# Optimization experiments

Hardware: AMD Instinct MI355X
Metric: run time of the kernel (lower is better)

Reference implementation:

```python
import jax, jax.numpy as jnp
import numpy as np

SHIFTS = [1, 3, 5, 7]
C = 16  # in_channels // 4
# -1 neighbor offsets for tmp1..tmp8 (dy, dx) in units of the dilation
OFFSETS = [(-1, -1), (-1, 0), (-1, 1), (0, 1), (1, 1), (1, 0), (1, -1), (0, -1)]


def setup_inputs() -> dict:
    key = jax.random.key(0)
    ks = jax.random.split(key, 32)
    d = {}
    d['cen'] = jax.random.normal(ks[0], (8, 64, 256, 256), jnp.float32)
    d['mas'] = jax.random.normal(ks[1], (8, 1, 256, 256), jnp.float32)
    d['in_conv_w'] = jax.random.normal(ks[2], (16, 64), jnp.float32) * 0.1
    d['in_conv_b'] = jax.random.normal(ks[3], (16,), jnp.float32) * 0.1
    for i, s in enumerate(SHIFTS):
        d[f'dw_w{s}'] = jax.random.normal(ks[4 + 2 * i], (16, 1, s, s), jnp.float32) * 0.1
        d[f'dw_b{s}'] = jax.random.normal(ks[5 + 2 * i], (16,), jnp.float32) * 0.1
    d['l1_w'] = jax.random.normal(ks[12], (4, 16, 4), jnp.float32) * 0.1
    d['l1_b'] = jax.random.normal(ks[13], (4, 16), jnp.float32) * 0.1
    d['l2_w'] = jax.random.normal(ks[14], (4, 16, 8), jnp.float32) * 0.1
    d['l2_b'] = jax.random.normal(ks[15], (4, 16), jnp.float32) * 0.1
    d['base_w'] = jax.random.normal(ks[16], (16, 4), jnp.float32) * 0.1
    d['bn_scale'] = jnp.ones((16,), jnp.float32)
    d['bn_bias'] = jnp.zeros((16,), jnp.float32)
    d['final_w'] = jax.random.normal(ks[17], (1, 16), jnp.float32) * 0.1
    d['final_b'] = jax.random.normal(ks[18], (1,), jnp.float32) * 0.1
    return d


def _dw_conv(x, w, b, pad):
    # depthwise conv, groups == channels
    y = jax.lax.conv_general_dilated(
        x, w, window_strides=(1, 1), padding=[(pad, pad), (pad, pad)],
        dimension_numbers=('NCHW', 'OIHW', 'NCHW'), feature_group_count=x.shape[1])
    return y + b[None, :, None, None]


def _shifted(x, dy, dx, d):
    # zero-padded shift: out(y,x) = in(y+dy, x+dx)
    H, W = x.shape[2], x.shape[3]
    p = jnp.pad(x, ((0, 0), (0, 0), (d, d), (d, d)))
    return p[:, :, d + dy:d + dy + H, d + dx:d + dx + W]


def _circ_shift(x, dw_w, dw_b, w1, b1, w2, b2, shift):
    x = _dw_conv(x, dw_w, dw_b, shift // 2)
    # tmp_k = x - x shifted by the k-th neighbor offset (dilation = shift)
    T = [x - _shifted(x, dy * shift, dx * shift, shift) for dy, dx in OFFSETS]
    # paired sums: S[k] = tmp_{k+1} + tmp_{k+5} (S repeats with period 4)
    S = [T[k] + T[k + 4] for k in range(4)]
    outs = []
    for k in range(8):  # fixed small structural loop
        feats = jnp.stack([S[(k + 1) % 4], S[(k + 3) % 4], S[(k + 2) % 4],
                           2.0 * T[(k + 4) % 8]], axis=2)  # (B,C,4,H,W)
        # grouped 1x1 conv (groups=C, 4C->C) == per-channel contraction over feature axis
        o = jnp.einsum('bcfhw,cf->bchw', feats, w1) + b1[None, :, None, None]
        outs.append(o * T[k])
    O = jnp.sort(jnp.stack(outs, axis=2), axis=2)  # (B,C,8,H,W) sorted over branch axis
    return jnp.einsum('bcfhw,cf->bchw', O, w2) + b2[None, :, None, None]


def reference(cen, mas, in_conv_w, in_conv_b, dw_w1, dw_b1, dw_w3, dw_b3,
              dw_w5, dw_b5, dw_w7, dw_b7, l1_w, l1_b, l2_w, l2_b,
              base_w, bn_scale, bn_bias, final_w, final_b):
    # in_conv: 1x1, in_channels -> C
    x = jnp.einsum('bihw,oi->bohw', cen, in_conv_w) + in_conv_b[None, :, None, None]
    dws = [(dw_w1, dw_b1), (dw_w3, dw_b3), (dw_w5, dw_b5), (dw_w7, dw_b7)]
    branches = [
        _circ_shift(x, dws[i][0], dws[i][1], l1_w[i], l1_b[i], l2_w[i], l2_b[i], SHIFTS[i])
        for i in range(len(SHIFTS))
    ]
    A = jnp.sort(jnp.stack(branches, axis=2), axis=2)  # (B,C,4,H,W)
    # out_conv: grouped 1x1 BaseConv (conv no-bias + BN(affine) + SiLU), then 1x1 -> 1, sigmoid
    y = jnp.einsum('bcfhw,cf->bchw', A, base_w)
    y = jax.nn.silu(y * bn_scale[None, :, None, None] + bn_bias[None, :, None, None])
    y = jnp.einsum('bchw,oc->bohw', y, final_w) + final_b[None, :, None, None]
    return jax.nn.sigmoid(y)
```

## Files before the change

### kernel.cpp

```cpp
#include <hip/hip_runtime.h>
#include <hip/hip_fp16.h>
#include <math.h>

#define HW 65536

typedef float v2f __attribute__((ext_vector_type(2), aligned(4)));
typedef _Float16 h2 __attribute__((ext_vector_type(2)));

__global__ __launch_bounds__(256, 8) void k_inconv(const float* __restrict__ cen,
                                                   const float* __restrict__ w,
                                                   const float* __restrict__ bias,
                                                   float* __restrict__ x) {
    int px = blockIdx.x * 256 + threadIdx.x;
    int b  = px >> 16;
    int hw = px & 65535;

    const float* src = cen + (long)(b * 64) * HW + hw;
    float acc[16];
#pragma unroll
    for (int o = 0; o < 16; o++) acc[o] = bias[o];

#pragma unroll 4
    for (int i = 0; i < 64; i++) {
        float v = src[(long)i * HW];
#pragma unroll
        for (int o = 0; o < 16; o++) acc[o] = fmaf(v, w[o * 64 + i], acc[o]);
    }
    float* dst = x + (long)(b * 16) * HW + hw;
#pragma unroll
    for (int o = 0; o < 16; o++) dst[(long)o * HW] = acc[o];
}

#define CEH(a, b) { h2 _t = __builtin_elementwise_min(a, b); \
                    b = __builtin_elementwise_max(a, b); a = _t; }

__device__ __forceinline__ void sort8_h2(h2* v) {
    CEH(v[0], v[1]); CEH(v[2], v[3]); CEH(v[4], v[5]); CEH(v[6], v[7]);
    CEH(v[0], v[2]); CEH(v[1], v[3]); CEH(v[4], v[6]); CEH(v[5], v[7]);
    CEH(v[1], v[2]); CEH(v[5], v[6]); CEH(v[0], v[4]); CEH(v[3], v[7]);
    CEH(v[1], v[5]); CEH(v[2], v[6]);
    CEH(v[1], v[4]); CEH(v[3], v[6]);
    CEH(v[2], v[4]); CEH(v[3], v[5]);
    CEH(v[3], v[4]);
}
__device__ __forceinline__ void sort4_h2(h2* v) {
    CEH(v[0], v[1]); CEH(v[2], v[3]); CEH(v[0], v[2]); CEH(v[1], v[3]); CEH(v[1], v[2]);
}

#define LXS 56
#define SS  48

__global__ __launch_bounds__(512, 4) void k_main(
    const float* __restrict__ x,
    const float* __restrict__ dw_w1, const float* __restrict__ dw_b1,
    const float* __restrict__ dw_w3, const float* __restrict__ dw_b3,
    const float* __restrict__ dw_w5, const float* __restrict__ dw_b5,
    const float* __restrict__ dw_w7, const float* __restrict__ dw_b7,
    const float* __restrict__ l1w, const float* __restrict__ l1b,
    const float* __restrict__ l2w, const float* __restrict__ l2b,
    const float* __restrict__ bw,  const float* __restrict__ bns,
    const float* __restrict__ bnb, __half* __restrict__ y16) {

    const int plane = blockIdx.y;
    const int c     = plane & 15;
    const int ty0   = (blockIdx.x >> 3) * 32;
    const int tx0   = (blockIdx.x & 7) * 32;
    const int tid   = threadIdx.x;

    __shared__ float lx[52 * LXS];
    __shared__ float lxs[4][46 * SS];

    const float* xp = x + (long)plane * HW;

    for (int i = tid; i < 52 * 52; i += 512) {
        int r  = i / 52;
        int cc = i - r * 52;
        int gy = ty0 - 10 + r, gx = tx0 - 10 + cc;
        float v = 0.f;
        if ((unsigned)gy < 256u && (unsigned)gx < 256u) v = xp[gy * 256 + gx];
        lx[r * LXS + cc] = v;
    }
    __syncthreads();

    const float* W7 = dw_w7 + c * 49;
    const float* W5 = dw_w5 + c * 25;
    const float* W3 = dw_w3 + c * 9;
    const float  W1 = dw_w1[c];
    const float  B1 = dw_b1[c], B3 = dw_b3[c], B5 = dw_b5[c], B7 = dw_b7[c];

    for (int u = tid; u < 46 * 23; u += 512) {
        int row = u / 23;
        int pc0 = (u - row * 23) * 2;
        v2f c7 = {0, 0}, c5 = {0, 0}, c3 = {0, 0}, c1 = {0, 0};
#pragma unroll
        for (int a = 0; a < 7; a++) {
            const float* rp = &lx[(row + a) * LXS + pc0];
            v2f q0 = *(const v2f*)rp;
            v2f q1 = *(const v2f*)(rp + 2);
            v2f q2 = *(const v2f*)(rp + 4);
            v2f q3 = *(const v2f*)(rp + 6);
            float v8 = rp[8];
            float v[9] = {q0.x, q0.y, q1.x, q1.y, q2.x, q2.y, q3.x, q3.y, v8};
#pragma unroll
            for (int bb = 0; bb < 7; bb++) {
                v2f vv = {v[bb], v[bb + 1]};
                c7 += vv * W7[a * 7 + bb];
            }
            if (a >= 1 && a <= 5) {
#pragma unroll
                for (int bb = 0; bb < 5; bb++) {
                    v2f vv = {v[bb + 1], v[bb + 2]};
                    c5 += vv * W5[(a - 1) * 5 + bb];
                }
            }
            if (a >= 2 && a <= 4) {
#pragma unroll
                for (int bb = 0; bb < 3; bb++) {
                    v2f vv = {v[bb + 2], v[bb + 3]};
                    c3 += vv * W3[(a - 2) * 3 + bb];
                }
            }
            if (a == 3) {
                v2f vv = {v[3], v[4]};
                c1 = vv * W1;
            }
        }
        int gy  = ty0 - 7 + row;
        int gx0 = tx0 - 7 + pc0;
        bool rin = ((unsigned)gy < 256u);
        bool in0 = rin && ((unsigned)gx0 < 256u);
        bool in1 = rin && ((unsigned)(gx0 + 1) < 256u);
        int o = row * SS + pc0;
        v2f s;
        s.x = in0 ? c1.x + B1 : 0.f; s.y = in1 ? c1.y + B1 : 0.f;
        *(v2f*)&lxs[0][o] = s;
        s.x = in0 ? c3.x + B3 : 0.f; s.y = in1 ? c3.y + B3 : 0.f;
        *(v2f*)&lxs[1][o] = s;
        s.x = in0 ? c5.x + B5 : 0.f; s.y = in1 ? c5.y + B5 : 0.f;
        *(v2f*)&lxs[2][o] = s;
        s.x = in0 ? c7.x + B7 : 0.f; s.y = in1 ? c7.y + B7 : 0.f;
        *(v2f*)&lxs[3][o] = s;
    }
    __syncthreads();

    const int ty  = tid >> 4;
    const int tx2 = (tid & 15) * 2;
    const int gy  = ty0 + ty, gx = tx0 + tx2;
    const int corner = ty * SS + tx2;

    v2f br[4];
#pragma unroll
    for (int i = 0; i < 4; i++) {
        const int s = 1 + 2 * i;
        const float* xs = lxs[i];
        v2f ctr = *(const v2f*)&xs[corner + 7 * SS + 7];
        v2f n0  = *(const v2f*)&xs[corner + (7 - s) * SS + (7 - s)];
        v2f n1  = *(const v2f*)&xs[corner + (7 - s) * SS + 7];
        v2f n2  = *(const v2f*)&xs[corner + (7 - s) * SS + (7 + s)];
        v2f n3  = *(const v2f*)&xs[corner + 7 * SS + (7 + s)];
        v2f n4  = *(const v2f*)&xs[corner + (7 + s) * SS + (7 + s)];
        v2f n5  = *(const v2f*)&xs[corner + (7 + s) * SS + 7];
        v2f n6  = *(const v2f*)&xs[corner + (7 + s) * SS + (7 - s)];
        v2f n7  = *(const v2f*)&xs[corner + 7 * SS + (7 - s)];

        v2f T[8];
        T[0] = ctr - n0; T[1] = ctr - n1; T[2] = ctr - n2; T[3] = ctr - n3;
        T[4] = ctr - n4; T[5] = ctr - n5; T[6] = ctr - n6; T[7] = ctr - n7;
        v2f S[4];
#pragma unroll
        for (int k = 0; k < 4; k++) S[k] = T[k] + T[k + 4];

        const float w10   = l1w[i * 64 + c * 4 + 0];
        const float w11   = l1w[i * 64 + c * 4 + 1];
        const float w12   = l1w[i * 64 + c * 4 + 2];
        const float w13x2 = 2.f * l1w[i * 64 + c * 4 + 3];
        const float bb1   = l1b[i * 16 + c];

        v2f R[4];
#pragma unroll
        for (int m = 0; m < 4; m++) {
            v2f r = S[(m + 2) & 3] * w12 + bb1;
            r = S[(m + 3) & 3] * w11 + r;
            r = S[(m + 1) & 3] * w10 + r;
            R[m] = r;
        }

        h2 h8[8];
#pragma unroll
        for (int k = 0; k < 8; k++) {
            v2f o = (T[(k + 4) & 7] * w13x2 + R[k & 3]) * T[k];
            h8[k] = __builtin_convertvector(o, h2);
        }
        sort8_h2(h8);

        v2f acc = {l2b[i * 16 + c], l2b[i * 16 + c]};
#pragma unroll
        for (int k = 0; k < 8; k++) {
            v2f ov = __builtin_convertvector(h8[k], v2f);
            acc += ov * l2w[i * 128 + c * 8 + k];
        }
        br[i] = acc;
    }

    h2 bh[4];
#pragma unroll
    for (int i = 0; i < 4; i++) bh[i] = __builtin_convertvector(br[i], h2);
    sort4_h2(bh);

    v2f yv = {0.f, 0.f};
#pragma unroll
    for (int i = 0; i < 4; i++) {
        v2f bv = __builtin_convertvector(bh[i], v2f);
        yv += bv * bw[c * 4 + i];
    }
    const float bsc = bns[c], bbi = bnb[c];
    float zx = fmaf(yv.x, bsc, bbi);
    float zy = fmaf(yv.y, bsc, bbi);
    float sx = zx / (1.f + __expf(-zx));
    float sy = zy / (1.f + __expf(-zy));
    *(__half2*)&y16[(long)plane * HW + gy * 256 + gx] = __floats2half2_rn(sx, sy);
}

__global__ __launch_bounds__(256) void k_final(const __half* __restrict__ y16,
                                               const float* __restrict__ fw,
                                               const float* __restrict__ fb,
                                               float* __restrict__ out) {
    long t  = (long)blockIdx.x * 256 + threadIdx.x;
    long p0 = t * 2;
    int  b  = (int)(p0 >> 16);
    int  hw = (int)(p0 & 65535);

    float accx = fb[0], accy = fb[0];
#pragma unroll
    for (int cc = 0; cc < 16; cc++) {
        __half2 h = *(const __half2*)(y16 + (long)(b * 16 + cc) * HW + hw);
        float2 v = __half22float2(h);
        float wv = fw[cc];
        accx = fmaf(v.x, wv, accx);
        accy = fmaf(v.y, wv, accy);
    }
    float2 r;
    r.x = 1.f / (1.f + __expf(-accx));
    r.y = 1.f / (1.f + __expf(-accy));
    *(float2*)(out + p0) = r;
}

extern "C" void kernel_launch(void* const* d_in, const int* in_sizes, int n_in,
                              void* d_out, int out_size, void* d_ws, size_t ws_size,
                              hipStream_t stream) {
    (void)in_sizes; (void)n_in; (void)out_size; (void)ws_size;
    const float* cen   = (const float*)d_in[0];
    const float* in_w  = (const float*)d_in[2];
    const float* in_b  = (const float*)d_in[3];
    const float* dw_w1 = (const float*)d_in[4];
    const float* dw_b1 = (const float*)d_in[5];
    const float* dw_w3 = (const float*)d_in[6];
    const float* dw_b3 = (const float*)d_in[7];
    const float* dw_w5 = (const float*)d_in[8];
    const float* dw_b5 = (const float*)d_in[9];
    const float* dw_w7 = (const float*)d_in[10];
    const float* dw_b7 = (const float*)d_in[11];
    const float* l1w   = (const float*)d_in[12];
    const float* l1b   = (const float*)d_in[13];
    const float* l2w   = (const float*)d_in[14];
    const float* l2b   = (const float*)d_in[15];
    const float* bw    = (const float*)d_in[16];
    const float* bns   = (const float*)d_in[17];
    const float* bnb   = (const float*)d_in[18];
    const float* fw    = (const float*)d_in[19];
    const float* fb    = (const float*)d_in[20];

    float*  xbuf = (float*)d_ws;
    __half* y16  = (__half*)(xbuf + (size_t)8 * 16 * HW);
    float*  out  = (float*)d_out;

    k_inconv<<<2048, 256, 0, stream>>>(cen, in_w, in_b, xbuf);
    k_main<<<dim3(64, 128), 512, 0, stream>>>(xbuf, dw_w1, dw_b1, dw_w3, dw_b3,
                                              dw_w5, dw_b5, dw_w7, dw_b7,
                                              l1w, l1b, l2w, l2b, bw, bns, bnb, y16);
    k_final<<<1024, 256, 0, stream>>>(y16, fw, fb, out);
}
```

Baseline: 394.4 us.

## Store intermediates in fp16 and run circ-shift math in packed half

```diff
diff --git a/kernel.cpp b/kernel.cpp
--- a/kernel.cpp
+++ b/kernel.cpp
@@ -7,28 +7,40 @@
 typedef float v2f __attribute__((ext_vector_type(2), aligned(4)));
 typedef _Float16 h2 __attribute__((ext_vector_type(2)));
 
-__global__ __launch_bounds__(256, 8) void k_inconv(const float* __restrict__ cen,
-                                                   const float* __restrict__ w,
-                                                   const float* __restrict__ bias,
-                                                   float* __restrict__ x) {
-    int px = blockIdx.x * 256 + threadIdx.x;
-    int b  = px >> 16;
-    int hw = px & 65535;
-
-    const float* src = cen + (long)(b * 64) * HW + hw;
-    float acc[16];
-#pragma unroll
-    for (int o = 0; o < 16; o++) acc[o] = bias[o];
+__global__ __launch_bounds__(256) void k_inconv(const float* __restrict__ cen,
+                                                const float* __restrict__ w,
+                                                const float* __restrict__ bias,
+                                                __half* __restrict__ xh) {
+    long t  = (long)blockIdx.x * 256 + threadIdx.x;
+    long p0 = t * 4;
+    int  b  = (int)(p0 >> 16);
+    int  hw = (int)(p0 & 65535);
+
+    const float4* src = (const float4*)(cen + ((long)b * 64) * HW + hw);
+    float4 acc[16];
+#pragma unroll
+    for (int o = 0; o < 16; o++) { float bv = bias[o]; acc[o] = make_float4(bv, bv, bv, bv); }
 
 #pragma unroll 4
     for (int i = 0; i < 64; i++) {
-        float v = src[(long)i * HW];
-#pragma unroll
-        for (int o = 0; o < 16; o++) acc[o] = fmaf(v, w[o * 64 + i], acc[o]);
-    }
-    float* dst = x + (long)(b * 16) * HW + hw;
-#pragma unroll
-    for (int o = 0; o < 16; o++) dst[(long)o * HW] = acc[o];
+        float4 v = src[(long)i * (HW / 4)];
+#pragma unroll
+        for (int o = 0; o < 16; o++) {
+            float wv = w[o * 64 + i];
+            acc[o].x = fmaf(v.x, wv, acc[o].x);
+            acc[o].y = fmaf(v.y, wv, acc[o].y);
+            acc[o].z = fmaf(v.z, wv, acc[o].z);
+            acc[o].w = fmaf(v.w, wv, acc[o].w);
+        }
+    }
+#pragma unroll
+    for (int o = 0; o < 16; o++) {
+        __half2 lo = __floats2half2_rn(acc[o].x, acc[o].y);
+        __half2 hi = __floats2half2_rn(acc[o].z, acc[o].w);
+        __half2* dst = (__half2*)(xh + ((long)(b * 16 + o)) * HW + hw);
+        dst[0] = lo;
+        dst[1] = hi;
+    }
 }
 
 #define CEH(a, b) { h2 _t = __builtin_elementwise_min(a, b); \
@@ -50,8 +62,8 @@
 #define LXS 56
 #define SS  48
 
-__global__ __launch_bounds__(512, 4) void k_main(
-    const float* __restrict__ x,
+__global__ __launch_bounds__(512, 8) void k_main(
+    const __half* __restrict__ xh,
     const float* __restrict__ dw_w1, const float* __restrict__ dw_b1,
     const float* __restrict__ dw_w3, const float* __restrict__ dw_b3,
     const float* __restrict__ dw_w5, const float* __restrict__ dw_b5,
@@ -67,17 +79,17 @@
     const int tx0   = (blockIdx.x & 7) * 32;
     const int tid   = threadIdx.x;
 
-    __shared__ float lx[52 * LXS];
-    __shared__ float lxs[4][46 * SS];
-
-    const float* xp = x + (long)plane * HW;
+    __shared__ float   lx[52 * LXS];
+    __shared__ _Float16 lxs[4][46 * SS];
+
+    const __half* xp = xh + (long)plane * HW;
 
     for (int i = tid; i < 52 * 52; i += 512) {
         int r  = i / 52;
         int cc = i - r * 52;
         int gy = ty0 - 10 + r, gx = tx0 - 10 + cc;
         float v = 0.f;
-        if ((unsigned)gy < 256u && (unsigned)gx < 256u) v = xp[gy * 256 + gx];
+        if ((unsigned)gy < 256u && (unsigned)gx < 256u) v = __half2float(xp[gy * 256 + gx]);
         lx[r * LXS + cc] = v;
     }
     __syncthreads();
@@ -133,13 +145,13 @@
         int o = row * SS + pc0;
         v2f s;
         s.x = in0 ? c1.x + B1 : 0.f; s.y = in1 ? c1.y + B1 : 0.f;
-        *(v2f*)&lxs[0][o] = s;
+        *(h2*)&lxs[0][o] = __builtin_convertvector(s, h2);
         s.x = in0 ? c3.x + B3 : 0.f; s.y = in1 ? c3.y + B3 : 0.f;
-        *(v2f*)&lxs[1][o] = s;
+        *(h2*)&lxs[1][o] = __builtin_convertvector(s, h2);
         s.x = in0 ? c5.x + B5 : 0.f; s.y = in1 ? c5.y + B5 : 0.f;
-        *(v2f*)&lxs[2][o] = s;
+        *(h2*)&lxs[2][o] = __builtin_convertvector(s, h2);
         s.x = in0 ? c7.x + B7 : 0.f; s.y = in1 ? c7.y + B7 : 0.f;
-        *(v2f*)&lxs[3][o] = s;
+        *(h2*)&lxs[3][o] = __builtin_convertvector(s, h2);
     }
     __syncthreads();
 
@@ -148,74 +160,74 @@
     const int gy  = ty0 + ty, gx = tx0 + tx2;
     const int corner = ty * SS + tx2;
 
-    v2f br[4];
+    h2 brh[4];
 #pragma unroll
     for (int i = 0; i < 4; i++) {
         const int s = 1 + 2 * i;
-        const float* xs = lxs[i];
-        v2f ctr = *(const v2f*)&xs[corner + 7 * SS + 7];
-        v2f n0  = *(const v2f*)&xs[corner + (7 - s) * SS + (7 - s)];
-        v2f n1  = *(const v2f*)&xs[corner + (7 - s) * SS + 7];
-        v2f n2  = *(const v2f*)&xs[corner + (7 - s) * SS + (7 + s)];
-        v2f n3  = *(const v2f*)&xs[corner + 7 * SS + (7 + s)];
-        v2f n4  = *(const v2f*)&xs[corner + (7 + s) * SS + (7 + s)];
-        v2f n5  = *(const v2f*)&xs[corner + (7 + s) * SS + 7];
-        v2f n6  = *(const v2f*)&xs[corner + (7 + s) * SS + (7 - s)];
-        v2f n7  = *(const v2f*)&xs[corner + 7 * SS + (7 - s)];
-
-        v2f T[8];
+        const _Float16* xs = lxs[i];
+        h2 ctr = *(const h2*)&xs[corner + 7 * SS + 7];
+        h2 n0  = *(const h2*)&xs[corner + (7 - s) * SS + (7 - s)];
+        h2 n1  = *(const h2*)&xs[corner + (7 - s) * SS + 7];
+        h2 n2  = *(const h2*)&xs[corner + (7 - s) * SS + (7 + s)];
+        h2 n3  = *(const h2*)&xs[corner + 7 * SS + (7 + s)];
+        h2 n4  = *(const h2*)&xs[corner + (7 + s) * SS + (7 + s)];
+        h2 n5  = *(const h2*)&xs[corner + (7 + s) * SS + 7];
+        h2 n6  = *(const h2*)&xs[corner + (7 + s) * SS + (7 - s)];
+        h2 n7  = *(const h2*)&xs[corner + 7 * SS + (7 - s)];
+
+        h2 T[8];
         T[0] = ctr - n0; T[1] = ctr - n1; T[2] = ctr - n2; T[3] = ctr - n3;
         T[4] = ctr - n4; T[5] = ctr - n5; T[6] = ctr - n6; T[7] = ctr - n7;
-        v2f S[4];
+        h2 S[4];
 #pragma unroll
         for (int k = 0; k < 4; k++) S[k] = T[k] + T[k + 4];
 
-        const float w10   = l1w[i * 64 + c * 4 + 0];
-        const float w11   = l1w[i * 64 + c * 4 + 1];
-        const float w12   = l1w[i * 64 + c * 4 + 2];
-        const float w13x2 = 2.f * l1w[i * 64 + c * 4 + 3];
-        const float bb1   = l1b[i * 16 + c];
-
-        v2f R[4];
+        const _Float16 w10   = (_Float16)l1w[i * 64 + c * 4 + 0];
+        const _Float16 w11   = (_Float16)l1w[i * 64 + c * 4 + 1];
+        const _Float16 w12   = (_Float16)l1w[i * 64 + c * 4 + 2];
+        const _Float16 w13x2 = (_Float16)(2.f * l1w[i * 64 + c * 4 + 3]);
+        const _Float16 bb1   = (_Float16)l1b[i * 16 + c];
+
+        const h2 vw10 = {w10, w10}, vw11 = {w11, w11}, vw12 = {w12, w12};
+        const h2 vw13 = {w13x2, w13x2}, vbb1 = {bb1, bb1};
+
+        h2 R[4];
 #pragma unroll
         for (int m = 0; m < 4; m++) {
-            v2f r = S[(m + 2) & 3] * w12 + bb1;
-            r = S[(m + 3) & 3] * w11 + r;
-            r = S[(m + 1) & 3] * w10 + r;
+            h2 r = S[(m + 2) & 3] * vw12 + vbb1;
+            r = S[(m + 3) & 3] * vw11 + r;
+            r = S[(m + 1) & 3] * vw10 + r;
             R[m] = r;
         }
 
         h2 h8[8];
 #pragma unroll
+        for (int k = 0; k < 8; k++)
+            h8[k] = (T[(k + 4) & 7] * vw13 + R[k & 3]) * T[k];
+        sort8_h2(h8);
+
+        _Float16 l2bh = (_Float16)l2b[i * 16 + c];
+        h2 acc = {l2bh, l2bh};
+#pragma unroll
         for (int k = 0; k < 8; k++) {
-            v2f o = (T[(k + 4) & 7] * w13x2 + R[k & 3]) * T[k];
-            h8[k] = __builtin_convertvector(o, h2);
-        }
-        sort8_h2(h8);
-
-        v2f acc = {l2b[i * 16 + c], l2b[i * 16 + c]};
-#pragma unroll
-        for (int k = 0; k < 8; k++) {
-            v2f ov = __builtin_convertvector(h8[k], v2f);
-            acc += ov * l2w[i * 128 + c * 8 + k];
-        }
-        br[i] = acc;
-    }
-
-    h2 bh[4];
-#pragma unroll
-    for (int i = 0; i < 4; i++) bh[i] = __builtin_convertvector(br[i], h2);
-    sort4_h2(bh);
-
-    v2f yv = {0.f, 0.f};
+            _Float16 wh = (_Float16)l2w[i * 128 + c * 8 + k];
+            h2 wv = {wh, wh};
+            acc = h8[k] * wv + acc;
+        }
+        brh[i] = acc;
+    }
+
+    sort4_h2(brh);
+    h2 yvh = {(_Float16)0.f, (_Float16)0.f};
 #pragma unroll
     for (int i = 0; i < 4; i++) {
-        v2f bv = __builtin_convertvector(bh[i], v2f);
-        yv += bv * bw[c * 4 + i];
+        _Float16 bwh = (_Float16)bw[c * 4 + i];
+        h2 bv = {bwh, bwh};
+        yvh = brh[i] * bv + yvh;
     }
     const float bsc = bns[c], bbi = bnb[c];
-    float zx = fmaf(yv.x, bsc, bbi);
-    float zy = fmaf(yv.y, bsc, bbi);
+    float zx = fmaf((float)yvh.x, bsc, bbi);
+    float zy = fmaf((float)yvh.y, bsc, bbi);
     float sx = zx / (1.f + __expf(-zx));
     float sy = zy / (1.f + __expf(-zy));
     *(__half2*)&y16[(long)plane * HW + gy * 256 + gx] = __floats2half2_rn(sx, sy);
@@ -270,12 +282,12 @@
     const float* fw    = (const float*)d_in[19];
     const float* fb    = (const float*)d_in[20];
 
-    float*  xbuf = (float*)d_ws;
-    __half* y16  = (__half*)(xbuf + (size_t)8 * 16 * HW);
-    float*  out  = (float*)d_out;
-
-    k_inconv<<<2048, 256, 0, stream>>>(cen, in_w, in_b, xbuf);
-    k_main<<<dim3(64, 128), 512, 0, stream>>>(xbuf, dw_w1, dw_b1, dw_w3, dw_b3,
+    __half* xh  = (__half*)d_ws;
+    __half* y16 = xh + (size_t)8 * 16 * HW;
+    float*  out = (float*)d_out;
+
+    k_inconv<<<512, 256, 0, stream>>>(cen, in_w, in_b, xh);
+    k_main<<<dim3(64, 128), 512, 0, stream>>>(xh, dw_w1, dw_b1, dw_w3, dw_b3,
                                               dw_w5, dw_b5, dw_w7, dw_b7,
                                               l1w, l1b, l2w, l2b, bw, bns, bnb, y16);
     k_final<<<1024, 256, 0, stream>>>(y16, fw, fb, out);
```

After: 431.8 us. 1.09x slower.
